# Kernel tuning notes

Hardware: AMD Instinct MI355X
Metric: run time of the kernel (lower is better)

Reference implementation:

```python
import jax, jax.numpy as jnp
from jax import lax
import numpy as np

B, L, D, V, NL = 16, 2048, 512, 512, 4


def layer_norm(x, g, b, eps=1e-5):
    m = jnp.mean(x, axis=-1, keepdims=True)
    v = jnp.var(x, axis=-1, keepdims=True)
    return (x - m) * lax.rsqrt(v + eps) * g + b


def setup_inputs() -> dict:
    key = jax.random.key(0)
    ks = jax.random.split(key, 8)
    s = 0.02
    rn = lambda k, shp: jax.random.normal(k, shp, jnp.float32) * s
    return {
        "x": jax.random.randint(ks[0], (B, L), 0, V),
        "ln_g": jnp.ones((NL, D), jnp.float32),
        "ln_b": jnp.zeros((NL, D), jnp.float32),
        "conv_w": rn(ks[1], (NL, D, D, 3)),
        "conv_b": jnp.zeros((NL, D), jnp.float32),
        "wg": rn(ks[2], (NL, D)),
        "bg": jnp.zeros((NL,), jnp.float32),
        "wout": rn(ks[3], (NL, D, D)),
        "bout": jnp.zeros((NL, D), jnp.float32),
        "fc_w": rn(ks[4], (NL, 2 * D, D)),
        "fc_b": jnp.zeros((NL, 2 * D), jnp.float32),
        "mo_w": rn(ks[5], (NL, D, D)),
        "mo_b": jnp.zeros((NL, D), jnp.float32),
        "lnf_g": jnp.ones((D,), jnp.float32),
        "lnf_b": jnp.zeros((D,), jnp.float32),
        "head_w": rn(ks[6], (V, D)),
        "head_b": jnp.zeros((V,), jnp.float32),
    }


def ssm(x, wg_l, bg_l, wout_l, bout_l):
    # scalar selective gate per token, broadcast over D (matches W_g: D->1)
    g = jax.nn.sigmoid(jnp.einsum('bld,d->bl', x, wg_l) + bg_l)[..., None]  # [B,L,1]

    def step(h, inp):
        xt, gt = inp  # [B,D], [B,1]
        h = (1.0 - gt) * h + gt * xt
        return h, h

    h0 = jnp.zeros((x.shape[0], x.shape[2]), x.dtype)
    _, hs = lax.scan(step, h0, (x.swapaxes(0, 1), g.swapaxes(0, 1)))
    hs = hs.swapaxes(0, 1)  # [B,L,D]
    return jnp.einsum('bld,ed->ble', hs, wout_l) + bout_l


def mamba_block(y, lg, lb, cw, cb, wg_l, bg_l, wo, bo, fw, fb, mw, mb):
    z = layer_norm(y, lg, lb)
    # Conv1d(k=3, pad=1) over time: NCH layout
    z = lax.conv_general_dilated(z.swapaxes(1, 2), cw, (1,), [(1, 1)],
                                 dimension_numbers=('NCH', 'OIH', 'NCH'))
    z = (z + cb[None, :, None]).swapaxes(1, 2)  # [B,L,D]
    z = ssm(z, wg_l, bg_l, wo, bo)
    gate, val = jnp.split(jnp.einsum('bld,ed->ble', z, fw) + fb, 2, axis=-1)
    z = jnp.einsum('bld,ed->ble', jax.nn.sigmoid(gate) * val, mw) + mb
    return y + z


def reference(x, ln_g, ln_b, conv_w, conv_b, wg, bg, wout, bout,
              fc_w, fc_b, mo_w, mo_b, lnf_g, lnf_b, head_w, head_b):
    y = jax.nn.one_hot(x, V, dtype=jnp.float32)  # unary embedding [B,L,V], V==D
    for i in range(NL):
        y = mamba_block(y, ln_g[i], ln_b[i], conv_w[i], conv_b[i], wg[i], bg[i],
                        wout[i], bout[i], fc_w[i], fc_b[i], mo_w[i], mo_b[i])
    y = layer_norm(y, lnf_g, lnf_b)
    logits = jnp.einsum('bld,vd->blv', y, head_w) + head_b
    return logits
```

## Files before the change

### kernel.cpp

```cpp
#include <hip/hip_runtime.h>
#include <stdint.h>

#define B_   16
#define L_   2048
#define D_   512
#define NL_  4
#define LP_  2050
#define TOK_ 32768
#define CH_  32
#define CL_  64

typedef unsigned short u16;
typedef unsigned int   u32;

typedef float f32x4 __attribute__((ext_vector_type(4)));
typedef short s16x8 __attribute__((ext_vector_type(8)));

#define Y_OFF     0ull
#define APAD_OFF  67108864ull
#define Z2_OFF    100696064ull
#define HS_OFF    134250496ull
#define G_OFF     167804928ull
#define B2_OFF    167936000ull
#define WCV_OFF   167952384ull
#define WMO_OFF   174243840ull
#define WHD_OFF   176340992ull
#define WOT_OFF   176865280ull
#define WFCB_OFF  178962432ull
#define WC_OFF    183156736ull
#define WS_NEED   187351040ull
#define ABUF_OFF  APAD_OFF
#define HLOC_OFF  (APAD_OFF + 1048576ull)
#define HST_OFF   (APAD_OFF + 2097152ull)

__device__ __forceinline__ u16 f2b(float f) {
    u32 u = __float_as_uint(f);
    return (u16)((u + 0x7fffu + ((u >> 16) & 1u)) >> 16);
}
__device__ __forceinline__ float b2f(u16 u) {
    return __uint_as_float(((u32)u) << 16);
}
__device__ __forceinline__ float sigmoidf_(float x) {
    return 1.f / (1.f + __expf(-x));
}

typedef const __attribute__((address_space(1))) u32 gas_u32;
typedef __attribute__((address_space(3))) u32 las_u32;
__device__ __forceinline__ void gload_lds16(const u16* g, u16* l) {
    __builtin_amdgcn_global_load_lds((gas_u32*)g, (las_u32*)l, 16, 0, 0);
}

__global__ void sentinel_kernel(float* o) { o[threadIdx.x] = 12345.f; }

__global__ void embed_kernel(const int* __restrict__ x, float* __restrict__ y) {
    const int idx = blockIdx.x * 256 + threadIdx.x;
    const int t  = idx >> 7;
    const int d0 = (idx & 127) * 4;
    const int tok = x[t];
    float4 v;
    v.x = (d0 + 0 == tok) ? 1.f : 0.f;
    v.y = (d0 + 1 == tok) ? 1.f : 0.f;
    v.z = (d0 + 2 == tok) ? 1.f : 0.f;
    v.w = (d0 + 3 == tok) ? 1.f : 0.f;
    ((float4*)y)[idx] = v;
}

__global__ void zeropad_kernel(u16* __restrict__ apad) {
    const int idx = blockIdx.x * 256 + threadIdx.x;
    const int b = idx >> 10;
    const int r = (idx >> 9) & 1;
    const int d = idx & 511;
    apad[((size_t)b * LP_ + (r ? (LP_ - 1) : 0)) * D_ + d] = 0;
}

__global__ __launch_bounds__(256)
void ln_kernel(const float* __restrict__ yin, const float* __restrict__ gw,
               const float* __restrict__ bw, u16* __restrict__ out, int pad_mode)
{
    const int lane = threadIdx.x & 63;
    const int wave = threadIdx.x >> 6;
    const int t = blockIdx.x * 4 + wave;
    const float4* yp = (const float4*)(yin + (size_t)t * D_);
    float4 f0 = yp[lane * 2 + 0];
    float4 f1 = yp[lane * 2 + 1];
    float s  = f0.x + f0.y + f0.z + f0.w + f1.x + f1.y + f1.z + f1.w;
    float ss = f0.x*f0.x + f0.y*f0.y + f0.z*f0.z + f0.w*f0.w
             + f1.x*f1.x + f1.y*f1.y + f1.z*f1.z + f1.w*f1.w;
#pragma unroll
    for (int off = 32; off > 0; off >>= 1) {
        s  += __shfl_xor(s, off);
        ss += __shfl_xor(ss, off);
    }
    const float mean = s * (1.f / D_);
    const float inv = rsqrtf(ss * (1.f / D_) - mean * mean + 1e-5f);
    size_t orow;
    if (pad_mode) orow = ((size_t)(t >> 11) * LP_ + (t & (L_ - 1)) + 1) * D_;
    else          orow = (size_t)t * D_;
    const int d0 = lane * 8;
    float vv[8] = {f0.x, f0.y, f0.z, f0.w, f1.x, f1.y, f1.z, f1.w};
    u32 pk[4];
#pragma unroll
    for (int j = 0; j < 4; ++j) {
        u16 lo = f2b((vv[2*j]   - mean) * inv * gw[d0 + 2*j]     + bw[d0 + 2*j]);
        u16 hi = f2b((vv[2*j+1] - mean) * inv * gw[d0 + 2*j + 1] + bw[d0 + 2*j + 1]);
        pk[j] = (u32)lo | ((u32)hi << 16);
    }
    *(uint4*)(out + orow + d0) = make_uint4(pk[0], pk[1], pk[2], pk[3]);
}

__global__ __launch_bounds__(256)
void gate_kernel(const u16* __restrict__ z, const float* __restrict__ wg,
                 const float* __restrict__ bg, float* __restrict__ g)
{
    const int lane = threadIdx.x & 63;
    const int wave = threadIdx.x >> 6;
    const int t = blockIdx.x * 4 + wave;
    const u16* zp = z + (size_t)t * D_ + lane * 8;
    ushort4 z0 = *(const ushort4*)zp;
    ushort4 z1 = *(const ushort4*)(zp + 4);
    const float4* wp = (const float4*)(wg + lane * 8);
    float4 w0 = wp[0], w1 = wp[1];
    float s = b2f(z0.x)*w0.x + b2f(z0.y)*w0.y + b2f(z0.z)*w0.z + b2f(z0.w)*w0.w
            + b2f(z1.x)*w1.x + b2f(z1.y)*w1.y + b2f(z1.z)*w1.z + b2f(z1.w)*w1.w;
#pragma unroll
    for (int off = 32; off > 0; off >>= 1) s += __shfl_xor(s, off);
    if (lane == 0) g[t] = sigmoidf_(s + bg[0]);
}

__global__ __launch_bounds__(256)
void scan1_kernel(const u16* __restrict__ z, const float* __restrict__ g,
                  float* __restrict__ Abuf, float* __restrict__ Hloc)
{
    const int idx = blockIdx.x * 256 + threadIdx.x;
    const int d = idx & 511;
    const int c = (idx >> 9) & (CH_ - 1);
    const int b = idx >> 14;
    const u16* zp = z + ((size_t)b * L_ + c * CL_) * D_ + d;
    const float* gp = g + b * L_ + c * CL_;
    float Aa = 1.f, h = 0.f;
#pragma unroll 4
    for (int s = 0; s < CL_; ++s) {
        const float gv = gp[s];
        const float a = 1.f - gv;
        h = a * h + gv * b2f(zp[(size_t)s * D_]);
        Aa *= a;
    }
    Abuf[idx] = Aa;
    Hloc[idx] = h;
}

__global__ __launch_bounds__(256)
void scan2_kernel(const float* __restrict__ Abuf, const float* __restrict__ Hloc,
                  float* __restrict__ Hstart)
{
    const int idx = blockIdx.x * 256 + threadIdx.x;
    const int d = idx & 511;
    const int b = idx >> 9;
    float H = 0.f;
#pragma unroll
    for (int c = 0; c < CH_; ++c) {
        const int o = (b * CH_ + c) * D_ + d;
        Hstart[o] = H;
        H = Abuf[o] * H + Hloc[o];
    }
}

__global__ __launch_bounds__(256)
void scan3_kernel(const u16* __restrict__ z, const float* __restrict__ g,
                  const float* __restrict__ Hstart, u16* __restrict__ hs)
{
    const int idx = blockIdx.x * 256 + threadIdx.x;
    const int d = idx & 511;
    const int c = (idx >> 9) & (CH_ - 1);
    const int b = idx >> 14;
    const u16* zp = z + ((size_t)b * L_ + c * CL_) * D_ + d;
    const float* gp = g + b * L_ + c * CL_;
    u16* hp = hs + ((size_t)b * L_ + c * CL_) * D_ + d;
    float h = Hstart[idx];
#pragma unroll 4
    for (int s = 0; s < CL_; ++s) {
        const float gv = gp[s];
        h = (1.f - gv) * h + gv * b2f(zp[(size_t)s * D_]);
        hp[(size_t)s * D_] = f2b(h);
    }
}

__global__ void cvt_kernel(const float* __restrict__ s, u16* __restrict__ d, int n) {
    const int idx = blockIdx.x * 256 + threadIdx.x;
    if (idx < n) d[idx] = f2b(s[idx]);
}
__global__ void conv_repack_kernel(const float* __restrict__ w, u16* __restrict__ o) {
    const int idx = blockIdx.x * 256 + threadIdx.x;
    const int tap = idx % 3;
    const int rest = idx / 3;
    const int i = rest & 511;
    const int oi = rest >> 9;
    o[(size_t)oi * 1536 + tap * 512 + i] = f2b(w[idx]);
}
__global__ void wo_transpose_kernel(const float* __restrict__ w, u16* __restrict__ o) {
    const int idx = blockIdx.x * 256 + threadIdx.x;
    const int d = idx & 511;
    const int e = (idx >> 9) & 511;
    const int l = idx >> 18;
    o[((size_t)(l * 512 + d) << 9) + e] = f2b(w[idx]);
}
__global__ __launch_bounds__(256)
void bias2_kernel(const float* __restrict__ fcw, const float* __restrict__ bout,
                  const float* __restrict__ fcb, float* __restrict__ b2)
{
    const int lane = threadIdx.x & 63;
    const int wave = threadIdx.x >> 6;
    const int f = blockIdx.x * 4 + wave;
    const int l = f >> 10;
    const float4* wp = (const float4*)(fcw + (size_t)f * 512 + lane * 8);
    const float4* bp = (const float4*)(bout + l * 512 + lane * 8);
    float4 w0 = wp[0], w1 = wp[1], v0 = bp[0], v1 = bp[1];
    float s = w0.x*v0.x + w0.y*v0.y + w0.z*v0.z + w0.w*v0.w
            + w1.x*v1.x + w1.y*v1.y + w1.z*v1.z + w1.w*v1.w;
#pragma unroll
    for (int off = 32; off > 0; off >>= 1) s += __shfl_xor(s, off);
    if (lane == 0) b2[f] = s + fcb[f];
}

#define BM 128
#define BN 128
#define BK 64

__global__ __launch_bounds__(256)
void gemm_bt(const u16* __restrict__ A, const u16* __restrict__ W,
             const float* __restrict__ bias, const float* __restrict__ residual,
             float* __restrict__ outF, u16* __restrict__ outB,
             int N, int K, int a_stride, int conv_mode,
             int az, int wz, int oz)
{
    __shared__ u16 As[BM][BK];
    __shared__ u16 Bs[BN][BK];

    const int tid  = threadIdx.x;
    const int lane = tid & 63;
    const int wave = tid >> 6;
    const int m0 = blockIdx.x * BM;
    const int n0 = blockIdx.y * BN;
    const int zb = blockIdx.z;

    size_t a_base;
    if (conv_mode) {
        const int b = m0 >> 11;
        const int l = m0 & (L_ - 1);
        a_base = ((size_t)b * LP_ + l) * D_;
    } else {
        a_base = (size_t)m0 * a_stride;
    }
    const u16* Ap = A + a_base + (size_t)zb * az;
    const u16* Wp = W + (size_t)n0 * K + (size_t)zb * wz;

    f32x4 acc[4][4];
#pragma unroll
    for (int i = 0; i < 4; ++i)
#pragma unroll
        for (int j = 0; j < 4; ++j)
#pragma unroll
            for (int r = 0; r < 4; ++r) acc[i][j][r] = 0.f;

    const int wm = (wave & 1) * 64;
    const int wn = (wave >> 1) * 64;
    const int srow_l = lane >> 3;
    const int scol   = ((lane & 7) ^ srow_l) << 3;
    u16* asBase = &As[0][0] + wave * 512;
    u16* bsBase = &Bs[0][0] + wave * 512;

    for (int k0 = 0; k0 < K; k0 += BK) {
        __syncthreads();
#pragma unroll
        for (int it = 0; it < 4; ++it) {
            const int row = it * 32 + wave * 8 + srow_l;
            gload_lds16(Ap + (size_t)row * a_stride + k0 + scol, asBase + it * 2048);
            gload_lds16(Wp + (size_t)row * K        + k0 + scol, bsBase + it * 2048);
        }
        __syncthreads();
        const int krow = lane & 15;
        const int sw = krow & 7;
#pragma unroll
        for (int kk = 0; kk < BK; kk += 32) {
            const int kcol = kk + ((lane >> 4) << 3);
            const int koff = (((kcol >> 3) ^ sw) << 3);
            s16x8 af[4], bfr[4];
#pragma unroll
            for (int i = 0; i < 4; ++i)
                af[i] = *(const s16x8*)(&As[wm + i * 16 + krow][koff]);
#pragma unroll
            for (int j = 0; j < 4; ++j)
                bfr[j] = *(const s16x8*)(&Bs[wn + j * 16 + krow][koff]);
#pragma unroll
            for (int i = 0; i < 4; ++i)
#pragma unroll
                for (int j = 0; j < 4; ++j)
                    acc[i][j] = __builtin_amdgcn_mfma_f32_16x16x32_bf16(af[i], bfr[j], acc[i][j], 0, 0, 0);
        }
    }

    const int col_l = lane & 15;
    const int row_q = (lane >> 4) * 4;
#pragma unroll
    for (int j = 0; j < 4; ++j) {
        const int col = n0 + wn + j * 16 + col_l;
        const float bv = bias ? bias[col] : 0.f;
#pragma unroll
        for (int i = 0; i < 4; ++i) {
#pragma unroll
            for (int r = 0; r < 4; ++r) {
                const int row = m0 + wm + i * 16 + row_q + r;
                const size_t off = (size_t)row * N + col + (size_t)zb * oz;
                float v = acc[i][j][r] + bv;
                if (residual) v += residual[off];
                if (outF) outF[off] = v;
                else      outB[off] = f2b(v);
            }
        }
    }
}

__global__ __launch_bounds__(256, 2)
void gemm_fc(const u16* __restrict__ A, const u16* __restrict__ Wc,
             const float* __restrict__ b2, u16* __restrict__ out)
{
    __shared__ u16 As[BM][BK];
    __shared__ u16 Bg[BN][BK];
    __shared__ u16 Bv[BN][BK];

    const int tid  = threadIdx.x;
    const int lane = tid & 63;
    const int wave = tid >> 6;
    const int m0 = blockIdx.x * BM;
    const int n0 = blockIdx.y * BN;

    const u16* Ap = A + (size_t)m0 * 512;
    const u16* Wg = Wc + (size_t)n0 * 512;
    const u16* Wv = Wc + (size_t)(n0 + 512) * 512;

    f32x4 accg[4][4], accv[4][4];
#pragma unroll
    for (int i = 0; i < 4; ++i)
#pragma unroll
        for (int j = 0; j < 4; ++j)
#pragma unroll
            for (int r = 0; r < 4; ++r) { accg[i][j][r] = 0.f; accv[i][j][r] = 0.f; }

    const int wm = (wave & 1) * 64;
    const int wn = (wave >> 1) * 64;
    const int srow_l = lane >> 3;
    const int scol   = ((lane & 7) ^ srow_l) << 3;
    u16* aB = &As[0][0] + wave * 512;
    u16* gB = &Bg[0][0] + wave * 512;
    u16* vB = &Bv[0][0] + wave * 512;

    for (int k0 = 0; k0 < 512; k0 += BK) {
        __syncthreads();
#pragma unroll
        for (int it = 0; it < 4; ++it) {
            const int row = it * 32 + wave * 8 + srow_l;
            gload_lds16(Ap + (size_t)row * 512 + k0 + scol, aB + it * 2048);
            gload_lds16(Wg + (size_t)row * 512 + k0 + scol, gB + it * 2048);
            gload_lds16(Wv + (size_t)row * 512 + k0 + scol, vB + it * 2048);
        }
        __syncthreads();
        const int krow = lane & 15;
        const int sw = krow & 7;
#pragma unroll
        for (int kk = 0; kk < BK; kk += 32) {
            const int kcol = kk + ((lane >> 4) << 3);
            const int koff = (((kcol >> 3) ^ sw) << 3);
            s16x8 af[4], bg[4], bv[4];
#pragma unroll
            for (int i = 0; i < 4; ++i)
                af[i] = *(const s16x8*)(&As[wm + i * 16 + krow][koff]);
#pragma unroll
            for (int j = 0; j < 4; ++j) {
                bg[j] = *(const s16x8*)(&Bg[wn + j * 16 + krow][koff]);
                bv[j] = *(const s16x8*)(&Bv[wn + j * 16 + krow][koff]);
            }
#pragma unroll
            for (int i = 0; i < 4; ++i)
#pragma unroll
                for (int j = 0; j < 4; ++j) {
                    accg[i][j] = __builtin_amdgcn_mfma_f32_16x16x32_bf16(af[i], bg[j], accg[i][j], 0, 0, 0);
                    accv[i][j] = __builtin_amdgcn_mfma_f32_16x16x32_bf16(af[i], bv[j], accv[i][j], 0, 0, 0);
                }
        }
    }

    const int col_l = lane & 15;
    const int row_q = (lane >> 4) * 4;
#pragma unroll
    for (int j = 0; j < 4; ++j) {
        const int col = n0 + wn + j * 16 + col_l;
        const float bg_ = b2[col];
        const float bv_ = b2[col + 512];
#pragma unroll
        for (int i = 0; i < 4; ++i) {
#pragma unroll
            for (int r = 0; r < 4; ++r) {
                const int row = m0 + wm + i * 16 + row_q + r;
                const float gval = sigmoidf_(accg[i][j][r] + bg_);
                const float vval = accv[i][j][r] + bv_;
                out[(size_t)row * 512 + col] = f2b(gval * vval);
            }
        }
    }
}

extern "C" void kernel_launch(void* const* d_in, const int* in_sizes, int n_in,
                              void* d_out, int out_size, void* d_ws, size_t ws_size,
                              hipStream_t stream)
{
    const int*   x      = (const int*)d_in[0];
    const float* ln_g   = (const float*)d_in[1];
    const float* ln_b   = (const float*)d_in[2];
    const float* conv_w = (const float*)d_in[3];
    const float* conv_b = (const float*)d_in[4];
    const float* wg     = (const float*)d_in[5];
    const float* bg     = (const float*)d_in[6];
    const float* wout   = (const float*)d_in[7];
    const float* bout   = (const float*)d_in[8];
    const float* fc_w   = (const float*)d_in[9];
    const float* fc_b   = (const float*)d_in[10];
    const float* mo_w   = (const float*)d_in[11];
    const float* mo_b   = (const float*)d_in[12];
    const float* lnf_g  = (const float*)d_in[13];
    const float* lnf_b  = (const float*)d_in[14];
    const float* head_w = (const float*)d_in[15];
    const float* head_b = (const float*)d_in[16];

    if (ws_size < WS_NEED) {
        sentinel_kernel<<<1, 256, 0, stream>>>((float*)d_out);
        return;
    }

    char* ws = (char*)d_ws;
    float* y    = (float*)(ws + Y_OFF);
    u16*   apad = (u16*)(ws + APAD_OFF);
    u16*   z2b  = (u16*)(ws + Z2_OFF);
    u16*   gv   = (u16*)(ws + Z2_OFF);
    u16*   hs   = (u16*)(ws + HS_OFF);
    float* gbuf = (float*)(ws + G_OFF);
    float* b2   = (float*)(ws + B2_OFF);
    float* Abuf = (float*)(ws + ABUF_OFF);
    float* Hloc = (float*)(ws + HLOC_OFF);
    float* Hst  = (float*)(ws + HST_OFF);
    u16*   wcv  = (u16*)(ws + WCV_OFF);
    u16*   wmo  = (u16*)(ws + WMO_OFF);
    u16*   whd  = (u16*)(ws + WHD_OFF);
    u16*   woT  = (u16*)(ws + WOT_OFF);
    u16*   wfcb = (u16*)(ws + WFCB_OFF);
    u16*   wc   = (u16*)(ws + WC_OFF);

    conv_repack_kernel<<<(NL_*512*512*3)/256, 256, 0, stream>>>(conv_w, wcv);
    cvt_kernel<<<(NL_*512*512)/256,  256, 0, stream>>>(mo_w,  wmo, NL_*512*512);
    cvt_kernel<<<(512*512)/256,      256, 0, stream>>>(head_w, whd, 512*512);
    cvt_kernel<<<(NL_*1024*512)/256, 256, 0, stream>>>(fc_w,  wfcb, NL_*1024*512);
    wo_transpose_kernel<<<(NL_*512*512)/256, 256, 0, stream>>>(wout, woT);
    gemm_bt<<<dim3(8, 4, 4), 256, 0, stream>>>(wfcb, woT, nullptr, nullptr,
            nullptr, wc, 512, 512, 512, 0, 1024*512, 512*512, 1024*512);
    bias2_kernel<<<(NL_*1024)/4, 256, 0, stream>>>(fc_w, bout, fc_b, b2);

    embed_kernel<<<(TOK_*D_/4)/256, 256, 0, stream>>>(x, y);

    for (int l = 0; l < NL_; ++l) {
        zeropad_kernel<<<64, 256, 0, stream>>>(apad);
        ln_kernel<<<TOK_/4, 256, 0, stream>>>(y, ln_g + l*512, ln_b + l*512, apad, 1);
        gemm_bt<<<dim3(256, 4), 256, 0, stream>>>(apad, wcv + (size_t)l*512*1536,
                conv_b + l*512, nullptr, nullptr, z2b, 512, 1536, 512, 1, 0, 0, 0);
        gate_kernel<<<TOK_/4, 256, 0, stream>>>(z2b, wg + l*512, bg + l, gbuf);
        scan1_kernel<<<(B_*CH_*D_)/256, 256, 0, stream>>>(z2b, gbuf, Abuf, Hloc);
        scan2_kernel<<<(B_*D_)/256, 256, 0, stream>>>(Abuf, Hloc, Hst);
        scan3_kernel<<<(B_*CH_*D_)/256, 256, 0, stream>>>(z2b, gbuf, Hst, hs);
        gemm_fc<<<dim3(256, 4), 256, 0, stream>>>(hs, wc + (size_t)l*1024*512,
                b2 + l*1024, gv);
        gemm_bt<<<dim3(256, 4), 256, 0, stream>>>(gv, wmo + (size_t)l*512*512,
                mo_b + l*512, y, y, nullptr, 512, 512, 512, 0, 0, 0, 0);
    }

    ln_kernel<<<TOK_/4, 256, 0, stream>>>(y, lnf_g, lnf_b, hs, 0);
    gemm_bt<<<dim3(256, 4), 256, 0, stream>>>(hs, whd, head_b, nullptr,
            (float*)d_out, nullptr, 512, 512, 512, 0, 0, 0, 0);

    (void)in_sizes; (void)n_in; (void)out_size;
}
```

Before: 1.114 ms.

## Switch GEMMs to 32x32 MFMA and fuse prep, pad and gate kernels

Replaces the 16x16x32 bf16 MFMA tiles in both GEMMs with 32x32x16 tiles (fewer LDS fragment loads per FLOP) and rewrites the accumulator and epilogue indexing to match. Merges the five weight-prep kernels into one launch, folds the zero-pad writes into extra LayerNorm blocks, and fuses the gate dot product into the first scan pass via shared memory. The aim is fewer kernel launches and less LDS traffic. The fused scan uses only 512 blocks, each thread handling two channels, which lowers parallelism in that pass.

After: 1.539 ms. +38.2%, slower.

```diff
diff --git a/kernel.cpp b/kernel.cpp
--- a/kernel.cpp
+++ b/kernel.cpp
@@ -13,8 +13,9 @@
 typedef unsigned short u16;
 typedef unsigned int   u32;
 
-typedef float f32x4 __attribute__((ext_vector_type(4)));
-typedef short s16x8 __attribute__((ext_vector_type(8)));
+typedef float f32x4  __attribute__((ext_vector_type(4)));
+typedef float f32x16 __attribute__((ext_vector_type(16)));
+typedef short s16x8  __attribute__((ext_vector_type(8)));
 
 #define Y_OFF     0ull
 #define APAD_OFF  67108864ull
@@ -65,18 +66,53 @@
     ((float4*)y)[idx] = v;
 }
 
-__global__ void zeropad_kernel(u16* __restrict__ apad) {
+#define PN1 3145728
+#define PN2 4194304
+#define PN3 4456448
+#define PN4 6553600
+#define PN5 7602176
+__global__ void prep_kernel(const float* __restrict__ conv_w, const float* __restrict__ mo_w,
+                            const float* __restrict__ head_w, const float* __restrict__ fc_w,
+                            const float* __restrict__ wout,
+                            u16* __restrict__ wcv, u16* __restrict__ wmo,
+                            u16* __restrict__ whd, u16* __restrict__ wfcb,
+                            u16* __restrict__ woT)
+{
     const int idx = blockIdx.x * 256 + threadIdx.x;
-    const int b = idx >> 10;
-    const int r = (idx >> 9) & 1;
-    const int d = idx & 511;
-    apad[((size_t)b * LP_ + (r ? (LP_ - 1) : 0)) * D_ + d] = 0;
+    if (idx < PN1) {
+        const int tap = idx % 3;
+        const int rest = idx / 3;
+        const int i = rest & 511;
+        const int oi = rest >> 9;
+        wcv[(size_t)oi * 1536 + tap * 512 + i] = f2b(conv_w[idx]);
+    } else if (idx < PN2) {
+        const int i = idx - PN1; wmo[i] = f2b(mo_w[i]);
+    } else if (idx < PN3) {
+        const int i = idx - PN2; whd[i] = f2b(head_w[i]);
+    } else if (idx < PN4) {
+        const int i = idx - PN3; wfcb[i] = f2b(fc_w[i]);
+    } else {
+        const int i = idx - PN4;
+        const int d = i & 511;
+        const int e = (i >> 9) & 511;
+        const int l = i >> 18;
+        woT[((size_t)(l * 512 + d) << 9) + e] = f2b(wout[i]);
+    }
 }
 
 __global__ __launch_bounds__(256)
 void ln_kernel(const float* __restrict__ yin, const float* __restrict__ gw,
                const float* __restrict__ bw, u16* __restrict__ out, int pad_mode)
 {
+    if (pad_mode && blockIdx.x >= TOK_ / 4) {
+        const int idx2 = (blockIdx.x - TOK_ / 4) * 256 + threadIdx.x;
+        const int b = idx2 >> 7;
+        const int r = (idx2 >> 6) & 1;
+        const int col = (idx2 & 63) * 8;
+        *(uint4*)(out + ((size_t)b * LP_ + (r ? (LP_ - 1) : 0)) * D_ + col) =
+            make_uint4(0, 0, 0, 0);
+        return;
+    }
     const int lane = threadIdx.x & 63;
     const int wave = threadIdx.x >> 6;
     const int t = blockIdx.x * 4 + wave;
@@ -109,44 +145,53 @@
 }
 
 __global__ __launch_bounds__(256)
-void gate_kernel(const u16* __restrict__ z, const float* __restrict__ wg,
-                 const float* __restrict__ bg, float* __restrict__ g)
-{
-    const int lane = threadIdx.x & 63;
-    const int wave = threadIdx.x >> 6;
-    const int t = blockIdx.x * 4 + wave;
-    const u16* zp = z + (size_t)t * D_ + lane * 8;
-    ushort4 z0 = *(const ushort4*)zp;
-    ushort4 z1 = *(const ushort4*)(zp + 4);
+void scan1g_kernel(const u16* __restrict__ z, const float* __restrict__ wg,
+                   const float* __restrict__ bg, float* __restrict__ g,
+                   float* __restrict__ Abuf, float* __restrict__ Hloc)
+{
+    __shared__ float gs[CL_];
+    const int bc = blockIdx.x;
+    const int b = bc >> 5;
+    const int c = bc & 31;
+    const int tid = threadIdx.x;
+    const int lane = tid & 63;
+    const int wave = tid >> 6;
+    const size_t zbase = ((size_t)b * L_ + c * CL_) * D_;
+
     const float4* wp = (const float4*)(wg + lane * 8);
-    float4 w0 = wp[0], w1 = wp[1];
-    float s = b2f(z0.x)*w0.x + b2f(z0.y)*w0.y + b2f(z0.z)*w0.z + b2f(z0.w)*w0.w
-            + b2f(z1.x)*w1.x + b2f(z1.y)*w1.y + b2f(z1.z)*w1.z + b2f(z1.w)*w1.w;
-#pragma unroll
-    for (int off = 32; off > 0; off >>= 1) s += __shfl_xor(s, off);
-    if (lane == 0) g[t] = sigmoidf_(s + bg[0]);
-}
-
-__global__ __launch_bounds__(256)
-void scan1_kernel(const u16* __restrict__ z, const float* __restrict__ g,
-                  float* __restrict__ Abuf, float* __restrict__ Hloc)
-{
-    const int idx = blockIdx.x * 256 + threadIdx.x;
-    const int d = idx & 511;
-    const int c = (idx >> 9) & (CH_ - 1);
-    const int b = idx >> 14;
-    const u16* zp = z + ((size_t)b * L_ + c * CL_) * D_ + d;
-    const float* gp = g + b * L_ + c * CL_;
-    float Aa = 1.f, h = 0.f;
+    const float4 w0 = wp[0], w1 = wp[1];
+    const float bgv = bg[0];
+#pragma unroll 4
+    for (int it = 0; it < 16; ++it) {
+        const int s = wave * 16 + it;
+        const u16* zp = z + zbase + (size_t)s * D_ + lane * 8;
+        ushort4 z0 = *(const ushort4*)zp;
+        ushort4 z1 = *(const ushort4*)(zp + 4);
+        float sum = b2f(z0.x)*w0.x + b2f(z0.y)*w0.y + b2f(z0.z)*w0.z + b2f(z0.w)*w0.w
+                  + b2f(z1.x)*w1.x + b2f(z1.y)*w1.y + b2f(z1.z)*w1.z + b2f(z1.w)*w1.w;
+#pragma unroll
+        for (int off = 32; off > 0; off >>= 1) sum += __shfl_xor(sum, off);
+        if (lane == 0) {
+            const float gv = sigmoidf_(sum + bgv);
+            gs[s] = gv;
+            g[b * L_ + c * CL_ + s] = gv;
+        }
+    }
+    __syncthreads();
+    const int d0 = tid;
+    const int d1 = tid + 256;
+    float h0 = 0.f, h1 = 0.f, Aa = 1.f;
 #pragma unroll 4
     for (int s = 0; s < CL_; ++s) {
-        const float gv = gp[s];
+        const float gv = gs[s];
         const float a = 1.f - gv;
-        h = a * h + gv * b2f(zp[(size_t)s * D_]);
+        h0 = a * h0 + gv * b2f(z[zbase + (size_t)s * D_ + d0]);
+        h1 = a * h1 + gv * b2f(z[zbase + (size_t)s * D_ + d1]);
         Aa *= a;
     }
-    Abuf[idx] = Aa;
-    Hloc[idx] = h;
+    const int o = bc * D_;
+    Abuf[o + d0] = Aa;  Abuf[o + d1] = Aa;
+    Hloc[o + d0] = h0;  Hloc[o + d1] = h1;
 }
 
 __global__ __launch_bounds__(256)
@@ -185,25 +230,6 @@
     }
 }
 
-__global__ void cvt_kernel(const float* __restrict__ s, u16* __restrict__ d, int n) {
-    const int idx = blockIdx.x * 256 + threadIdx.x;
-    if (idx < n) d[idx] = f2b(s[idx]);
-}
-__global__ void conv_repack_kernel(const float* __restrict__ w, u16* __restrict__ o) {
-    const int idx = blockIdx.x * 256 + threadIdx.x;
-    const int tap = idx % 3;
-    const int rest = idx / 3;
-    const int i = rest & 511;
-    const int oi = rest >> 9;
-    o[(size_t)oi * 1536 + tap * 512 + i] = f2b(w[idx]);
-}
-__global__ void wo_transpose_kernel(const float* __restrict__ w, u16* __restrict__ o) {
-    const int idx = blockIdx.x * 256 + threadIdx.x;
-    const int d = idx & 511;
-    const int e = (idx >> 9) & 511;
-    const int l = idx >> 18;
-    o[((size_t)(l * 512 + d) << 9) + e] = f2b(w[idx]);
-}
 __global__ __launch_bounds__(256)
 void bias2_kernel(const float* __restrict__ fcw, const float* __restrict__ bout,
                   const float* __restrict__ fcb, float* __restrict__ b2)
@@ -226,6 +252,8 @@
 #define BN 128
 #define BK 64
 
+#define MFMA32(a, b, c) __builtin_amdgcn_mfma_f32_32x32x16_bf16(a, b, c, 0, 0, 0)
+
 __global__ __launch_bounds__(256)
 void gemm_bt(const u16* __restrict__ A, const u16* __restrict__ W,
              const float* __restrict__ bias, const float* __restrict__ residual,
@@ -254,13 +282,13 @@
     const u16* Ap = A + a_base + (size_t)zb * az;
     const u16* Wp = W + (size_t)n0 * K + (size_t)zb * wz;
 
-    f32x4 acc[4][4];
-#pragma unroll
-    for (int i = 0; i < 4; ++i)
-#pragma unroll
-        for (int j = 0; j < 4; ++j)
-#pragma unroll
-            for (int r = 0; r < 4; ++r) acc[i][j][r] = 0.f;
+    f32x16 acc[2][2];
+#pragma unroll
+    for (int i = 0; i < 2; ++i)
+#pragma unroll
+        for (int j = 0; j < 2; ++j)
+#pragma unroll
+            for (int r = 0; r < 16; ++r) acc[i][j][r] = 0.f;
 
     const int wm = (wave & 1) * 64;
     const int wn = (wave >> 1) * 64;
@@ -269,6 +297,10 @@
     u16* asBase = &As[0][0] + wave * 512;
     u16* bsBase = &Bs[0][0] + wave * 512;
 
+    const int lrow  = lane & 31;
+    const int khalf = (lane >> 5) * 8;
+    const int sw    = lane & 7;
+
     for (int k0 = 0; k0 < K; k0 += BK) {
         __syncthreads();
 #pragma unroll
@@ -278,38 +310,32 @@
             gload_lds16(Wp + (size_t)row * K        + k0 + scol, bsBase + it * 2048);
         }
         __syncthreads();
-        const int krow = lane & 15;
-        const int sw = krow & 7;
-#pragma unroll
-        for (int kk = 0; kk < BK; kk += 32) {
-            const int kcol = kk + ((lane >> 4) << 3);
+#pragma unroll
+        for (int kk = 0; kk < BK; kk += 16) {
+            const int kcol = kk + khalf;
             const int koff = (((kcol >> 3) ^ sw) << 3);
-            s16x8 af[4], bfr[4];
-#pragma unroll
-            for (int i = 0; i < 4; ++i)
-                af[i] = *(const s16x8*)(&As[wm + i * 16 + krow][koff]);
-#pragma unroll
-            for (int j = 0; j < 4; ++j)
-                bfr[j] = *(const s16x8*)(&Bs[wn + j * 16 + krow][koff]);
-#pragma unroll
-            for (int i = 0; i < 4; ++i)
-#pragma unroll
-                for (int j = 0; j < 4; ++j)
-                    acc[i][j] = __builtin_amdgcn_mfma_f32_16x16x32_bf16(af[i], bfr[j], acc[i][j], 0, 0, 0);
-        }
-    }
-
-    const int col_l = lane & 15;
-    const int row_q = (lane >> 4) * 4;
-#pragma unroll
-    for (int j = 0; j < 4; ++j) {
-        const int col = n0 + wn + j * 16 + col_l;
+            s16x8 af0 = *(const s16x8*)(&As[wm + lrow][koff]);
+            s16x8 af1 = *(const s16x8*)(&As[wm + 32 + lrow][koff]);
+            s16x8 bf0 = *(const s16x8*)(&Bs[wn + lrow][koff]);
+            s16x8 bf1 = *(const s16x8*)(&Bs[wn + 32 + lrow][koff]);
+            acc[0][0] = MFMA32(af0, bf0, acc[0][0]);
+            acc[0][1] = MFMA32(af0, bf1, acc[0][1]);
+            acc[1][0] = MFMA32(af1, bf0, acc[1][0]);
+            acc[1][1] = MFMA32(af1, bf1, acc[1][1]);
+        }
+    }
+
+    const int col_l = lane & 31;
+    const int rbase = (lane >> 5) * 4;
+#pragma unroll
+    for (int j = 0; j < 2; ++j) {
+        const int col = n0 + wn + j * 32 + col_l;
         const float bv = bias ? bias[col] : 0.f;
 #pragma unroll
-        for (int i = 0; i < 4; ++i) {
-#pragma unroll
-            for (int r = 0; r < 4; ++r) {
-                const int row = m0 + wm + i * 16 + row_q + r;
+        for (int i = 0; i < 2; ++i) {
+#pragma unroll
+            for (int r = 0; r < 16; ++r) {
+                const int row = m0 + wm + i * 32 + (r & 3) + 8 * (r >> 2) + rbase;
                 const size_t off = (size_t)row * N + col + (size_t)zb * oz;
                 float v = acc[i][j][r] + bv;
                 if (residual) v += residual[off];
@@ -338,13 +364,13 @@
     const u16* Wg = Wc + (size_t)n0 * 512;
     const u16* Wv = Wc + (size_t)(n0 + 512) * 512;
 
-    f32x4 accg[4][4], accv[4][4];
-#pragma unroll
-    for (int i = 0; i < 4; ++i)
-#pragma unroll
-        for (int j = 0; j < 4; ++j)
-#pragma unroll
-            for (int r = 0; r < 4; ++r) { accg[i][j][r] = 0.f; accv[i][j][r] = 0.f; }
+    f32x16 accg[2][2], accv[2][2];
+#pragma unroll
+    for (int i = 0; i < 2; ++i)
+#pragma unroll
+        for (int j = 0; j < 2; ++j)
+#pragma unroll
+            for (int r = 0; r < 16; ++r) { accg[i][j][r] = 0.f; accv[i][j][r] = 0.f; }
 
     const int wm = (wave & 1) * 64;
     const int wn = (wave >> 1) * 64;
@@ -354,6 +380,10 @@
     u16* gB = &Bg[0][0] + wave * 512;
     u16* vB = &Bv[0][0] + wave * 512;
 
+    const int lrow  = lane & 31;
+    const int khalf = (lane >> 5) * 8;
+    const int sw    = lane & 7;
+
     for (int k0 = 0; k0 < 512; k0 += BK) {
         __syncthreads();
 #pragma unroll
@@ -364,43 +394,39 @@
             gload_lds16(Wv + (size_t)row * 512 + k0 + scol, vB + it * 2048);
         }
         __syncthreads();
-        const int krow = lane & 15;
-        const int sw = krow & 7;
-#pragma unroll
-        for (int kk = 0; kk < BK; kk += 32) {
-            const int kcol = kk + ((lane >> 4) << 3);
+#pragma unroll
+        for (int kk = 0; kk < BK; kk += 16) {
+            const int kcol = kk + khalf;
             const int koff = (((kcol >> 3) ^ sw) << 3);
-            s16x8 af[4], bg[4], bv[4];
-#pragma unroll
-            for (int i = 0; i < 4; ++i)
-                af[i] = *(const s16x8*)(&As[wm + i * 16 + krow][koff]);
-#pragma unroll
-            for (int j = 0; j < 4; ++j) {
-                bg[j] = *(const s16x8*)(&Bg[wn + j * 16 + krow][koff]);
-                bv[j] = *(const s16x8*)(&Bv[wn + j * 16 + krow][koff]);
-            }
-#pragma unroll
-            for (int i = 0; i < 4; ++i)
-#pragma unroll
-                for (int j = 0; j < 4; ++j) {
-                    accg[i][j] = __builtin_amdgcn_mfma_f32_16x16x32_bf16(af[i], bg[j], accg[i][j], 0, 0, 0);
-                    accv[i][j] = __builtin_amdgcn_mfma_f32_16x16x32_bf16(af[i], bv[j], accv[i][j], 0, 0, 0);
-                }
-        }
-    }
-
-    const int col_l = lane & 15;
-    const int row_q = (lane >> 4) * 4;
-#pragma unroll
-    for (int j = 0; j < 4; ++j) {
-        const int col = n0 + wn + j * 16 + col_l;
+            s16x8 af0 = *(const s16x8*)(&As[wm + lrow][koff]);
+            s16x8 af1 = *(const s16x8*)(&As[wm + 32 + lrow][koff]);
+            s16x8 bg0 = *(const s16x8*)(&Bg[wn + lrow][koff]);
+            s16x8 bg1 = *(const s16x8*)(&Bg[wn + 32 + lrow][koff]);
+            s16x8 bv0 = *(const s16x8*)(&Bv[wn + lrow][koff]);
+            s16x8 bv1 = *(const s16x8*)(&Bv[wn + 32 + lrow][koff]);
+            accg[0][0] = MFMA32(af0, bg0, accg[0][0]);
+            accg[0][1] = MFMA32(af0, bg1, accg[0][1]);
+            accg[1][0] = MFMA32(af1, bg0, accg[1][0]);
+            accg[1][1] = MFMA32(af1, bg1, accg[1][1]);
+            accv[0][0] = MFMA32(af0, bv0, accv[0][0]);
+            accv[0][1] = MFMA32(af0, bv1, accv[0][1]);
+            accv[1][0] = MFMA32(af1, bv0, accv[1][0]);
+            accv[1][1] = MFMA32(af1, bv1, accv[1][1]);
+        }
+    }
+
+    const int col_l = lane & 31;
+    const int rbase = (lane >> 5) * 4;
+#pragma unroll
+    for (int j = 0; j < 2; ++j) {
+        const int col = n0 + wn + j * 32 + col_l;
         const float bg_ = b2[col];
         const float bv_ = b2[col + 512];
 #pragma unroll
-        for (int i = 0; i < 4; ++i) {
-#pragma unroll
-            for (int r = 0; r < 4; ++r) {
-                const int row = m0 + wm + i * 16 + row_q + r;
+        for (int i = 0; i < 2; ++i) {
+#pragma unroll
+            for (int r = 0; r < 16; ++r) {
+                const int row = m0 + wm + i * 32 + (r & 3) + 8 * (r >> 2) + rbase;
                 const float gval = sigmoidf_(accg[i][j][r] + bg_);
                 const float vval = accv[i][j][r] + bv_;
                 out[(size_t)row * 512 + col] = f2b(gval * vval);
@@ -454,11 +480,8 @@
     u16*   wfcb = (u16*)(ws + WFCB_OFF);
     u16*   wc   = (u16*)(ws + WC_OFF);
 
-    conv_repack_kernel<<<(NL_*512*512*3)/256, 256, 0, stream>>>(conv_w, wcv);
-    cvt_kernel<<<(NL_*512*512)/256,  256, 0, stream>>>(mo_w,  wmo, NL_*512*512);
-    cvt_kernel<<<(512*512)/256,      256, 0, stream>>>(head_w, whd, 512*512);
-    cvt_kernel<<<(NL_*1024*512)/256, 256, 0, stream>>>(fc_w,  wfcb, NL_*1024*512);
-    wo_transpose_kernel<<<(NL_*512*512)/256, 256, 0, stream>>>(wout, woT);
+    prep_kernel<<<PN5 / 256, 256, 0, stream>>>(conv_w, mo_w, head_w, fc_w, wout,
+                                               wcv, wmo, whd, wfcb, woT);
     gemm_bt<<<dim3(8, 4, 4), 256, 0, stream>>>(wfcb, woT, nullptr, nullptr,
             nullptr, wc, 512, 512, 512, 0, 1024*512, 512*512, 1024*512);
     bias2_kernel<<<(NL_*1024)/4, 256, 0, stream>>>(fc_w, bout, fc_b, b2);
@@ -466,12 +489,10 @@
     embed_kernel<<<(TOK_*D_/4)/256, 256, 0, stream>>>(x, y);
 
     for (int l = 0; l < NL_; ++l) {
-        zeropad_kernel<<<64, 256, 0, stream>>>(apad);
-        ln_kernel<<<TOK_/4, 256, 0, stream>>>(y, ln_g + l*512, ln_b + l*512, apad, 1);
+        ln_kernel<<<TOK_/4 + 8, 256, 0, stream>>>(y, ln_g + l*512, ln_b + l*512, apad, 1);
         gemm_bt<<<dim3(256, 4), 256, 0, stream>>>(apad, wcv + (size_t)l*512*1536,
                 conv_b + l*512, nullptr, nullptr, z2b, 512, 1536, 512, 1, 0, 0, 0);
-        gate_kernel<<<TOK_/4, 256, 0, stream>>>(z2b, wg + l*512, bg + l, gbuf);
-        scan1_kernel<<<(B_*CH_*D_)/256, 256, 0, stream>>>(z2b, gbuf, Abuf, Hloc);
+        scan1g_kernel<<<B_*CH_, 256, 0, stream>>>(z2b, wg + l*512, bg + l, gbuf, Abuf, Hloc);
         scan2_kernel<<<(B_*D_)/256, 256, 0, stream>>>(Abuf, Hloc, Hst);
         scan3_kernel<<<(B_*CH_*D_)/256, 256, 0, stream>>>(z2b, gbuf, Hst, hs);
         gemm_fc<<<dim3(256, 4), 256, 0, stream>>>(hs, wc + (size_t)l*1024*512,
```
